# Kernel tuning notes

Measured on AMD Instinct MI355X. Metric: run time of the kernel, lower is better.

The kernel has to match this reference:

```python
import jax, jax.numpy as jnp
import numpy as np

NH = 10      # number of nearest source neighbors per target (init arg nh)
EPS = 1e-10  # numerical guard for inverse-distance weights


def setup_inputs() -> dict:
    key = jax.random.key(0)
    k1, k2 = jax.random.split(key)
    # x: [B, N_source, C] field values at source points
    x = jax.random.normal(k1, (8, 4096, 8), dtype=jnp.float32)
    # rel: [N_target, N_source, 2] relative (lon, lat) offsets target->source
    rel = jax.random.normal(k2, (16384, 4096, 2), dtype=jnp.float32)
    return {"x": x, "rel": rel}


def reference(x, rel):
    # input_dropout has p=0 -> identity, so it is omitted.
    # Pairwise Euclidean distances: [N_target, N_source]
    d = jnp.sqrt(jnp.sum(rel * rel, axis=-1))
    # nh nearest sources per target (top_k of negated distances)
    neg_topd, idx = jax.lax.top_k(-d, NH)          # idx: [T, NH]
    dist = -neg_topd                               # [T, NH]
    # inverse-distance weights, normalized over the NH neighbors
    w = 1.0 / (dist + EPS)
    w = w / jnp.sum(w, axis=-1, keepdims=True)     # [T, NH]
    # gather neighbor values: [B, T, NH, C]
    vals = jnp.take(x, idx, axis=1)
    # weighted sum over neighbors -> [B, T, C]
    return jnp.einsum('tk,btkc->btc', w, vals)
```

## Files before the change

kernel.cpp:

```cpp
#include <hip/hip_runtime.h>

#define NH 10
#define NB 8
#define NC 8
#define NT 16384
#define NS 4096
#define EPSW 1e-10f
#define FINF 3.402823466e+38f

__global__ __launch_bounds__(256) void knn_interp_kernel(
    const float* __restrict__ x,
    const float* __restrict__ rel,
    float* __restrict__ out)
{
    const int lane = threadIdx.x & 63;
    const int wave = threadIdx.x >> 6;
    const int t = blockIdx.x * 4 + wave;

    float v[NH];
    int   id[NH];
#pragma unroll
    for (int k = 0; k < NH; ++k) { v[k] = FINF; id[k] = 0x7FFFFFFF; }

    const float4* relrow = (const float4*)(rel + (size_t)t * (NS * 2));

#pragma unroll 4
    for (int j = 0; j < (NS / 2 / 64); ++j) {
        const int f4i = j * 64 + lane;
        float4 f = relrow[f4i];
        const int s0 = f4i * 2;

        float d2a = f.x * f.x + f.y * f.y;
        float d2b = f.z * f.z + f.w * f.w;

        if (d2a < v[NH - 1]) {
            float tv = d2a; int ti = s0;
#pragma unroll
            for (int k = 0; k < NH; ++k) {
                bool c = tv < v[k];
                float nv = c ? tv : v[k];
                float mv = c ? v[k] : tv;
                int   ni = c ? ti : id[k];
                int   mi = c ? id[k] : ti;
                v[k] = nv; id[k] = ni; tv = mv; ti = mi;
            }
        }
        if (d2b < v[NH - 1]) {
            float tv = d2b; int ti = s0 + 1;
#pragma unroll
            for (int k = 0; k < NH; ++k) {
                bool c = tv < v[k];
                float nv = c ? tv : v[k];
                float mv = c ? v[k] : tv;
                int   ni = c ? ti : id[k];
                int   mi = c ? id[k] : ti;
                v[k] = nv; id[k] = ni; tv = mv; ti = mi;
            }
        }
    }

    float rd[NH];
    int   ridx[NH];
#pragma unroll
    for (int r = 0; r < NH; ++r) {
        unsigned long long key =
            ((unsigned long long)__float_as_uint(v[0]) << 32) | (unsigned)id[0];
        unsigned long long m = key;
#pragma unroll
        for (int o = 32; o > 0; o >>= 1) {
            unsigned long long other = __shfl_xor(m, o, 64);
            m = (other < m) ? other : m;
        }
        rd[r]   = __uint_as_float((unsigned)(m >> 32));
        ridx[r] = (int)(unsigned)(m & 0xFFFFFFFFull);

        bool won = (key == m);
#pragma unroll
        for (int k = 0; k < NH - 1; ++k) {
            v[k]  = won ? v[k + 1]  : v[k];
            id[k] = won ? id[k + 1] : id[k];
        }
        v[NH - 1]  = won ? FINF : v[NH - 1];
        id[NH - 1] = won ? 0x7FFFFFFF : id[NH - 1];
    }

    float w[NH];
    float wsum = 0.f;
#pragma unroll
    for (int r = 0; r < NH; ++r) {
        float d = sqrtf(rd[r]);
        w[r] = 1.0f / (d + EPSW);
        wsum += w[r];
    }
    const float inv = 1.0f / wsum;

    const int b = lane >> 3;
    const int c = lane & 7;
    const float* xb = x + ((size_t)b * NS) * NC + c;
    float acc = 0.f;
#pragma unroll
    for (int r = 0; r < NH; ++r) {
        acc += w[r] * xb[(size_t)ridx[r] * NC];
    }
    out[((size_t)b * NT + t) * NC + c] = acc * inv;
}

extern "C" void kernel_launch(void* const* d_in, const int* in_sizes, int n_in,
                              void* d_out, int out_size, void* d_ws, size_t ws_size,
                              hipStream_t stream) {
    const float* x   = (const float*)d_in[0];
    const float* rel = (const float*)d_in[1];
    float* out = (float*)d_out;

    dim3 grid(NT / 4);
    dim3 block(256);
    knn_interp_kernel<<<grid, block, 0, stream>>>(x, rel, out);
}
```

Baseline: 693.8 us.

## Branchless med3 top-k insertion with register double-buffered nontemporal loads

Replaces the divergent, serial compare-swap top-k insertion with a branchless parallel insert that uses fmed3 and independent per-slot compares, so every candidate is inserted unconditionally. The streaming loop now double-buffers four float4 loads per lane, prefetching the next chunk while the current one is processed, and uses nontemporal loads for the large rel tensor. This trades more ALU work per element, since there is no early-out skip, for removing wave divergence and hiding memory latency in what is a bandwidth-bound stream.

```diff
diff --git a/kernel.cpp b/kernel.cpp
--- a/kernel.cpp
+++ b/kernel.cpp
@@ -7,6 +7,24 @@
 #define NS 4096
 #define EPSW 1e-10f
 #define FINF 3.402823466e+38f
+
+typedef float float4n __attribute__((ext_vector_type(4)));
+
+__device__ __forceinline__ void insert1(float t, int ti, float v[NH], int id[NH]) {
+    bool c[NH];
+#pragma unroll
+    for (int k = 0; k < NH; ++k) c[k] = t < v[k];
+    float nv[NH]; int ni[NH];
+    nv[0] = c[0] ? t : v[0];
+    ni[0] = c[0] ? ti : id[0];
+#pragma unroll
+    for (int k = 1; k < NH; ++k) {
+        nv[k] = __builtin_amdgcn_fmed3f(t, v[k - 1], v[k]);
+        ni[k] = c[k - 1] ? id[k - 1] : (c[k] ? ti : id[k]);
+    }
+#pragma unroll
+    for (int k = 0; k < NH; ++k) { v[k] = nv[k]; id[k] = ni[k]; }
+}
 
 __global__ __launch_bounds__(256) void knn_interp_kernel(
     const float* __restrict__ x,
@@ -22,41 +40,37 @@
 #pragma unroll
     for (int k = 0; k < NH; ++k) { v[k] = FINF; id[k] = 0x7FFFFFFF; }
 
-    const float4* relrow = (const float4*)(rel + (size_t)t * (NS * 2));
+    const float4n* relrow = (const float4n*)(rel + (size_t)t * (NS * 2));
 
-#pragma unroll 4
-    for (int j = 0; j < (NS / 2 / 64); ++j) {
-        const int f4i = j * 64 + lane;
-        float4 f = relrow[f4i];
-        const int s0 = f4i * 2;
+    float4n cur[4];
+#pragma unroll
+    for (int u = 0; u < 4; ++u)
+        cur[u] = __builtin_nontemporal_load(&relrow[u * 64 + lane]);
 
-        float d2a = f.x * f.x + f.y * f.y;
-        float d2b = f.z * f.z + f.w * f.w;
-
-        if (d2a < v[NH - 1]) {
-            float tv = d2a; int ti = s0;
+#pragma unroll 1
+    for (int j = 0; j < 7; ++j) {
+        float4n nxt[4];
 #pragma unroll
-            for (int k = 0; k < NH; ++k) {
-                bool c = tv < v[k];
-                float nv = c ? tv : v[k];
-                float mv = c ? v[k] : tv;
-                int   ni = c ? ti : id[k];
-                int   mi = c ? id[k] : ti;
-                v[k] = nv; id[k] = ni; tv = mv; ti = mi;
-            }
+        for (int u = 0; u < 4; ++u)
+            nxt[u] = __builtin_nontemporal_load(&relrow[(j + 1) * 256 + u * 64 + lane]);
+#pragma unroll
+        for (int u = 0; u < 4; ++u) {
+            const int f4i = j * 256 + u * 64 + lane;
+            float d2a = cur[u].x * cur[u].x + cur[u].y * cur[u].y;
+            float d2b = cur[u].z * cur[u].z + cur[u].w * cur[u].w;
+            insert1(d2a, f4i * 2,     v, id);
+            insert1(d2b, f4i * 2 + 1, v, id);
         }
-        if (d2b < v[NH - 1]) {
-            float tv = d2b; int ti = s0 + 1;
 #pragma unroll
-            for (int k = 0; k < NH; ++k) {
-                bool c = tv < v[k];
-                float nv = c ? tv : v[k];
-                float mv = c ? v[k] : tv;
-                int   ni = c ? ti : id[k];
-                int   mi = c ? id[k] : ti;
-                v[k] = nv; id[k] = ni; tv = mv; ti = mi;
-            }
-        }
+        for (int u = 0; u < 4; ++u) cur[u] = nxt[u];
+    }
+#pragma unroll
+    for (int u = 0; u < 4; ++u) {
+        const int f4i = 7 * 256 + u * 64 + lane;
+        float d2a = cur[u].x * cur[u].x + cur[u].y * cur[u].y;
+        float d2b = cur[u].z * cur[u].z + cur[u].w * cur[u].w;
+        insert1(d2a, f4i * 2,     v, id);
+        insert1(d2b, f4i * 2 + 1, v, id);
     }
 
     float rd[NH];
```

After: 662.1 us. 1.05x faster.
